# Kernel optimization log

Hardware: AMD Instinct MI355X
Metric: run time of the kernel (lower is better)

## Reference

```python
import jax, jax.numpy as jnp
import numpy as np

BS, L, HIDDEN = 4, 2048, 1024
H, HD, R = 16, 64, 4


def setup_inputs() -> dict:
    key = jax.random.key(0)
    k1, k2, k3, k4 = jax.random.split(key, 4)
    hidden_states = jax.random.normal(k1, (BS, L, HIDDEN), dtype=jnp.float32)
    scale = np.float32(1.0 / np.sqrt(HIDDEN))
    Wk = jax.random.normal(k2, (HIDDEN, H * HD), dtype=jnp.float32) * scale
    bk = jnp.zeros((H * HD,), jnp.float32)
    Wv = jax.random.normal(k3, (HIDDEN, H * HD), dtype=jnp.float32) * scale
    bv = jnp.zeros((H * HD,), jnp.float32)
    xavier = np.float32(np.sqrt(2.0 / (H + HD)))  # xavier_normal_ for (H, HD)
    ReadingHead = jax.random.normal(k4, (H, HD), dtype=jnp.float32) * xavier
    bidirection_weight = jnp.full((H, 2 * R), 1.0 / (2 * R), jnp.float32)
    return dict(hidden_states=hidden_states, Wk=Wk, bk=bk, Wv=Wv, bv=bv,
                ReadingHead=ReadingHead, bidirection_weight=bidirection_weight)


def _shift_step(carry, x):
    # carry: [bs, R, H] int32 registers; x = (valid [bs, H] bool, slot0 scalar int32)
    v, s = x
    bs, r, nh = carry.shape
    shifted = jnp.concatenate([jnp.broadcast_to(s, (bs, 1, nh)).astype(carry.dtype),
                               carry[:, :-1, :]], axis=1)
    new = jnp.where(v[:, None, :], shifted, carry)
    return new, new


def _forward_regs(valid):
    # valid: [bs, L, H] bool -> register index map [bs, L, R, H]
    bs, length, nh = valid.shape
    init = jnp.zeros((bs, R, nh), jnp.int32)  # position 0 registers are 0
    xs = (jnp.moveaxis(valid[:, 1:, :], 1, 0), jnp.arange(1, length, dtype=jnp.int32))
    _, ys = jax.lax.scan(_shift_step, init, xs)
    regs = jnp.concatenate([init[None], ys], axis=0)  # [L, bs, R, H]
    return jnp.moveaxis(regs, 0, 1)


def _backward_regs(valid):
    # valid: [bs, L, H] bool -> register index map [bs, L, R, H]
    bs, length, nh = valid.shape
    last = jnp.where(valid[:, length - 1, :], jnp.int32(length - 1), jnp.int32(0))
    init = jnp.zeros((bs, R, nh), jnp.int32).at[:, 0, :].set(last)  # position L-1
    # scan over positions 1..L-2 in reverse; slot0 at position l is l+1
    xs = (jnp.moveaxis(valid[:, 1:length - 1, :], 1, 0),
          jnp.arange(2, length, dtype=jnp.int32))
    _, ys = jax.lax.scan(_shift_step, init, xs, reverse=True)
    regs = jnp.concatenate([jnp.zeros((1, bs, R, nh), jnp.int32), ys, init[None]], axis=0)
    return jnp.moveaxis(regs, 0, 1)


def _gather_regs(V, regs):
    # V: [bs, L, H, hd]; regs: [bs, L, R, H] -> [bs, H, L, R, hd]
    bs, length, nh, hd = V.shape
    Vt = jnp.moveaxis(V, 2, 1)                       # [bs, H, L, hd]
    idx = jnp.moveaxis(regs, 3, 1).reshape(bs, nh, length * R)
    g = jnp.take_along_axis(Vt, idx[..., None], axis=2)  # [bs, H, L*R, hd]
    return g.reshape(bs, nh, length, R, hd)


def reference(hidden_states, Wk, bk, Wv, bv, ReadingHead, bidirection_weight):
    bs, length, _ = hidden_states.shape
    K1 = jax.nn.relu(hidden_states @ Wk + bk).reshape(bs, length, H, HD)
    V1 = jax.nn.relu(hidden_states @ Wv + bv).reshape(bs, length, H, HD)
    dot = jnp.einsum('blhd,hd->blh', K1, ReadingHead)
    valid = dot > 0.5  # attn_var == 'default' branch
    reg_f = _forward_regs(valid)
    reg_b = _backward_regs(valid)
    Vf = _gather_regs(V1, reg_f)  # [bs, H, L, R, hd]
    Vb = _gather_regs(V1, reg_b)
    out = (jnp.einsum('bhlrd,hr->blhd', Vf, bidirection_weight[:, :R])
           + jnp.einsum('bhlrd,hr->blhd', Vb, bidirection_weight[:, R:]))
    return out.reshape(bs, length, H * HD)
```

## Files before the change

### kernel.cpp

```cpp
#include <hip/hip_runtime.h>
#include <hip/hip_bf16.h>
#include <stdint.h>

#define BS   4
#define LSEQ 2048
#define HID  1024
#define NH   16
#define HD   64
#define M_TOT (BS * LSEQ)
#define NKV   (NH * HD)

typedef __attribute__((ext_vector_type(8))) short short8x;
typedef __attribute__((ext_vector_type(4))) float f32x4;

__device__ __forceinline__ float relu_f(float x) { return x > 0.0f ? x : 0.0f; }

__device__ __forceinline__ ushort bf16_rne(float f) {
    uint32_t x = __float_as_uint(f);
    return (ushort)((x + 0x7FFFu + ((x >> 16) & 1u)) >> 16);
}
__device__ __forceinline__ float bf16_to_f(ushort h) {
    return __uint_as_float((uint32_t)h << 16);
}

__device__ __forceinline__ void gload_lds16(const void* g, void* l) {
    typedef __attribute__((address_space(1))) const uint32_t GU;
    typedef __attribute__((address_space(3))) uint32_t LU;
    __builtin_amdgcn_global_load_lds((GU*)g, (LU*)l, 16, 0, 0);
}


__global__ __launch_bounds__(256) void split_A(const float* __restrict__ A,
                                               ushort* __restrict__ hi,
                                               ushort* __restrict__ lo)
{
    int i = blockIdx.x * 256 + threadIdx.x;
    float4 v = ((const float4*)A)[i];
    ushort4 h, l;
    h.x = bf16_rne(v.x); l.x = bf16_rne(v.x - bf16_to_f(h.x));
    h.y = bf16_rne(v.y); l.y = bf16_rne(v.y - bf16_to_f(h.y));
    h.z = bf16_rne(v.z); l.z = bf16_rne(v.z - bf16_to_f(h.z));
    h.w = bf16_rne(v.w); l.w = bf16_rne(v.w - bf16_to_f(h.w));
    ((ushort4*)hi)[i] = h;
    ((ushort4*)lo)[i] = l;
}

__global__ __launch_bounds__(256) void split_WT(const float* __restrict__ W,
                                                ushort* __restrict__ hiT,
                                                ushort* __restrict__ loT)
{
    __shared__ float t[64][65];
    const int k0 = blockIdx.x * 64, n0 = blockIdx.y * 64;
    const int tid = threadIdx.x;
#pragma unroll
    for (int it = 0; it < 4; ++it) {
        int r = it * 16 + (tid >> 4);
        int c = (tid & 15) * 4;
        float4 v = *(const float4*)&W[(size_t)(k0 + r) * NKV + n0 + c];
        t[r][c] = v.x; t[r][c + 1] = v.y; t[r][c + 2] = v.z; t[r][c + 3] = v.w;
    }
    __syncthreads();
    int n  = tid >> 2;
    int kc = (tid & 3) * 16;
    ushort hb[16], lb[16];
#pragma unroll
    for (int j = 0; j < 16; ++j) {
        float f = t[kc + j][n];
        ushort h = bf16_rne(f);
        hb[j] = h;
        lb[j] = bf16_rne(f - bf16_to_f(h));
    }
    size_t o = (size_t)(n0 + n) * 1024 + k0 + kc;
    *(uint4*)&hiT[o]     = *(uint4*)&hb[0];
    *(uint4*)&hiT[o + 8] = *(uint4*)&hb[8];
    *(uint4*)&loT[o]     = *(uint4*)&lb[0];
    *(uint4*)&loT[o + 8] = *(uint4*)&lb[8];
}

__global__ __launch_bounds__(256, 2) void mfma_gemm(
    const ushort* __restrict__ Ahi, const ushort* __restrict__ Alo,
    const ushort* __restrict__ WvhiT, const ushort* __restrict__ WvloT,
    const ushort* __restrict__ WkhiT, const ushort* __restrict__ WkloT,
    const float* __restrict__ bv, const float* __restrict__ bk,
    const float* __restrict__ RH,
    float* __restrict__ V1, unsigned char* __restrict__ validB)
{
    __shared__ ushort As[128 * 64];
    __shared__ ushort Bsh[128 * 64];

    const int tid  = threadIdx.x;
    const int lane = tid & 63;
    const int wv   = tid >> 6;
    const int wm   = wv >> 1;
    const int wn   = wv & 1;
    const int bm   = blockIdx.x;
    const bool kpath = (blockIdx.y >= 8);
    const int bn   = blockIdx.y & 7;

    const ushort* WT_hi = kpath ? WkhiT : WvhiT;
    const ushort* WT_lo = kpath ? WkloT : WvloT;
    const float*  bias  = kpath ? bk : bv;

    f32x4 acc[4][4];
    const f32x4 z = {0.f, 0.f, 0.f, 0.f};
#pragma unroll
    for (int i = 0; i < 4; ++i)
#pragma unroll
        for (int j = 0; j < 4; ++j) acc[i][j] = z;

    for (int ks = 0; ks < 48; ++ks) {
        const int seg = ks >> 4;
        const int k0  = (ks & 15) << 6;
        const ushort* Aseg = (seg == 1) ? Alo : Ahi;
        const ushort* Wseg = (seg == 2) ? WT_lo : WT_hi;

#pragma unroll
        for (int it = 0; it < 4; ++it) {
            int f = it * 256 + tid;
            int r = f >> 3, c = f & 7;
            const ushort* asrc = Aseg + (size_t)(bm * 128 + r) * 1024 + k0 + ((c ^ (r & 7)) << 3);
            gload_lds16(asrc, &As[(size_t)(it * 256 + wv * 64) * 8]);
        }
#pragma unroll
        for (int it = 0; it < 4; ++it) {
            int f = it * 256 + tid;
            int r = f >> 3, c = f & 7;
            const ushort* bsrc = Wseg + (size_t)(bn * 128 + r) * 1024 + k0 + ((c ^ (r & 7)) << 3);
            gload_lds16(bsrc, &Bsh[(size_t)(it * 256 + wv * 64) * 8]);
        }
        __syncthreads();

        short8x a[4][2], b[4][2];
#pragma unroll
        for (int mi = 0; mi < 4; ++mi)
#pragma unroll
            for (int k2 = 0; k2 < 2; ++k2) {
                int row = wm * 64 + mi * 16 + (lane & 15);
                int ch  = k2 * 4 + (lane >> 4);
                a[mi][k2] = *(const short8x*)((const char*)As + row * 128 + ((ch ^ (row & 7)) << 4));
            }
#pragma unroll
        for (int ni = 0; ni < 4; ++ni)
#pragma unroll
            for (int k2 = 0; k2 < 2; ++k2) {
                int row = wn * 64 + ni * 16 + (lane & 15);
                int ch  = k2 * 4 + (lane >> 4);
                b[ni][k2] = *(const short8x*)((const char*)Bsh + row * 128 + ((ch ^ (row & 7)) << 4));
            }

#pragma unroll
        for (int k2 = 0; k2 < 2; ++k2)
#pragma unroll
            for (int mi = 0; mi < 4; ++mi)
#pragma unroll
                for (int ni = 0; ni < 4; ++ni)
                    acc[mi][ni] = __builtin_amdgcn_mfma_f32_16x16x32_bf16(
                        a[mi][k2], b[ni][k2], acc[mi][ni], 0, 0, 0);
        __syncthreads();
    }

    if (!kpath) {
#pragma unroll
        for (int mi = 0; mi < 4; ++mi)
#pragma unroll
            for (int ni = 0; ni < 4; ++ni) {
                int row0 = bm * 128 + wm * 64 + mi * 16 + (lane >> 4) * 4;
                int col  = bn * 128 + wn * 64 + ni * 16 + (lane & 15);
                float bc = bias[col];
#pragma unroll
                for (int r = 0; r < 4; ++r)
                    V1[(size_t)(row0 + r) * NKV + col] = relu_f(acc[mi][ni][r] + bc);
            }
    } else {
        const int head = bn * 2 + wn;
        float rhw[4], bcs[4];
#pragma unroll
        for (int ni = 0; ni < 4; ++ni) {
            int ch = ni * 16 + (lane & 15);
            rhw[ni] = RH[head * HD + ch];
            bcs[ni] = bias[bn * 128 + wn * 64 + ch];
        }
#pragma unroll
        for (int mi = 0; mi < 4; ++mi) {
            float s[4];
#pragma unroll
            for (int r = 0; r < 4; ++r) {
                float v = 0.f;
#pragma unroll
                for (int ni = 0; ni < 4; ++ni)
                    v += relu_f(acc[mi][ni][r] + bcs[ni]) * rhw[ni];
                s[r] = v;
            }
#pragma unroll
            for (int m = 1; m < 16; m <<= 1)
#pragma unroll
                for (int r = 0; r < 4; ++r)
                    s[r] += __shfl_xor(s[r], m);
            if ((lane & 15) == 0) {
#pragma unroll
                for (int r = 0; r < 4; ++r) {
                    int grow = bm * 128 + wm * 64 + mi * 16 + (lane >> 4) * 4 + r;
                    int bb = grow >> 11, ll = grow & 2047;
                    validB[((size_t)bb * NH + head) * LSEQ + ll] = (s[r] > 0.5f) ? 1 : 0;
                }
            }
        }
    }
}

__global__ __launch_bounds__(256) void scan_kernel(
    const unsigned char* __restrict__ validB,
    short* __restrict__ idxb)
{
    const int bh = blockIdx.x;
    const int b  = bh >> 4;
    const int h  = bh & 15;
    const unsigned char* v = validB + ((size_t)b * NH + h) * LSEQ;

    __shared__ uint64_t words[LSEQ / 64];

    const int tid  = threadIdx.x;
    const int lane = tid & 63;
    const int wv   = tid >> 6;

#pragma unroll
    for (int it = 0; it < LSEQ / 256; ++it) {
        int p = it * 256 + wv * 64 + lane;
        uint64_t m = __ballot(v[p] != 0);
        if (lane == 0) {
            if ((p >> 6) == 0) m &= ~1ull;
            words[p >> 6] = m;
        }
    }
    __syncthreads();

#pragma unroll
    for (int it = 0; it < LSEQ / 256; ++it) {
        int l = it * 256 + tid;
        ushort f[4] = {0, 0, 0, 0};
        ushort g[4] = {0, 0, 0, 0};
        if (l > 0) {
            {
                int wi = l >> 6, bi = l & 63;
                uint64_t m = words[wi] & ((bi == 63) ? ~0ull : ((2ull << bi) - 1));
                int cnt = 0;
                while (cnt < 4) {
                    if (m == 0) { if (wi == 0) break; m = words[--wi]; continue; }
                    int p = 63 - __clzll(m);
                    f[cnt++] = (ushort)(wi * 64 + p);
                    m &= ~(1ull << p);
                }
            }
            {
                int wi = l >> 6, bi = l & 63;
                uint64_t m = words[wi] & (~0ull << bi);
                int cnt = 0;
                while (cnt < 4) {
                    if (m == 0) { if (wi == (LSEQ / 64) - 1) break; m = words[++wi]; continue; }
                    int p = __ffsll((long long)m) - 1;
                    int pos = wi * 64 + p;
                    g[cnt++] = (ushort)((pos >= LSEQ - 1) ? (LSEQ - 1) : (pos + 1));
                    m &= m - 1;
                }
            }
        }
        uint4 pk;
        pk.x = (uint32_t)f[0] | ((uint32_t)f[1] << 16);
        pk.y = (uint32_t)f[2] | ((uint32_t)f[3] << 16);
        pk.z = (uint32_t)g[0] | ((uint32_t)g[1] << 16);
        pk.w = (uint32_t)g[2] | ((uint32_t)g[3] << 16);
        *(uint4*)(idxb + (((size_t)(b * LSEQ + l)) * NH + h) * 8) = pk;
    }
}

__global__ __launch_bounds__(256) void gather_kernel(
    const float* __restrict__ V1,
    const short* __restrict__ idxb,
    const float* __restrict__ bw,
    float* __restrict__ out)
{
    int wid  = (blockIdx.x * 256 + threadIdx.x) >> 6;
    int lane = threadIdx.x & 63;
    int gr   = wid >> 4;
    int h    = wid & 15;
    int b    = gr >> 11;

    const ushort4* ip = (const ushort4*)(idxb + ((size_t)gr * NH + h) * 8);
    ushort4 i0 = ip[0];
    ushort4 i1 = ip[1];

    const float* wp    = bw + h * 8;
    const float* vbase = V1 + (size_t)b * LSEQ * NKV + h * HD + lane;

    float acc = wp[0] * vbase[(size_t)i0.x * NKV] + wp[1] * vbase[(size_t)i0.y * NKV] +
                wp[2] * vbase[(size_t)i0.z * NKV] + wp[3] * vbase[(size_t)i0.w * NKV] +
                wp[4] * vbase[(size_t)i1.x * NKV] + wp[5] * vbase[(size_t)i1.y * NKV] +
                wp[6] * vbase[(size_t)i1.z * NKV] + wp[7] * vbase[(size_t)i1.w * NKV];

    out[(size_t)gr * NKV + h * HD + lane] = acc;
}

extern "C" void kernel_launch(void* const* d_in, const int* in_sizes, int n_in,
                              void* d_out, int out_size, void* d_ws, size_t ws_size,
                              hipStream_t stream)
{
    const float* hs = (const float*)d_in[0];
    const float* Wk = (const float*)d_in[1];
    const float* bk = (const float*)d_in[2];
    const float* Wv = (const float*)d_in[3];
    const float* bv = (const float*)d_in[4];
    const float* RH = (const float*)d_in[5];
    const float* bw = (const float*)d_in[6];
    float* out = (float*)d_out;

    char* ws = (char*)d_ws;
    size_t o = 0;
    float* V1      = (float*)(ws + o);  o += (size_t)M_TOT * NKV * 4;
    ushort* Ahi    = (ushort*)(ws + o); o += (size_t)M_TOT * HID * 2;
    ushort* Alo    = (ushort*)(ws + o); o += (size_t)M_TOT * HID * 2;
    ushort* WvhiT  = (ushort*)(ws + o); o += (size_t)HID * NKV * 2;
    ushort* WvloT  = (ushort*)(ws + o); o += (size_t)HID * NKV * 2;
    ushort* WkhiT  = (ushort*)(ws + o); o += (size_t)HID * NKV * 2;
    ushort* WkloT  = (ushort*)(ws + o); o += (size_t)HID * NKV * 2;
    unsigned char* validB = (unsigned char*)(ws + o); o += (size_t)BS * NH * LSEQ;
    short* idxb    = (short*)(ws + o);  o += (size_t)M_TOT * NH * 8 * 2;

    split_A<<<(M_TOT * HID / 4) / 256, 256, 0, stream>>>(hs, Ahi, Alo);
    split_WT<<<dim3(16, 16), 256, 0, stream>>>(Wv, WvhiT, WvloT);
    split_WT<<<dim3(16, 16), 256, 0, stream>>>(Wk, WkhiT, WkloT);
    mfma_gemm<<<dim3(M_TOT / 128, 16), 256, 0, stream>>>(
        Ahi, Alo, WvhiT, WvloT, WkhiT, WkloT, bv, bk, RH, V1, validB);
    scan_kernel<<<BS * NH, 256, 0, stream>>>(validB, idxb);
    gather_kernel<<<(M_TOT * NH) / 4, 256, 0, stream>>>(V1, idxb, bw, out);
}
```

Measured before the change: 242.9 us.

## Rewrite bf16x3 GEMM as 256x256 double-buffered pipelined kernel; merge split kernels

Each GEMM workgroup now has 512 threads computing a 256x256 tile, up from 128x128. Shared memory is double-buffered, and global-to-LDS loads for the next K step are interleaved with MFMA phases using barriers, setprio and explicit vmcnt waits. This is meant to hide memory latency and raise data reuse per loaded tile. The three split/transpose launches are also folded into a single prep kernel to cut launch overhead. In exchange, LDS use and register pressure rise (acc grows to 8x4 per wave), and the grid shrinks to 256 workgroups, so occupancy and load balance may suffer.

```diff
diff --git a/kernel.cpp b/kernel.cpp
--- a/kernel.cpp
+++ b/kernel.cpp
@@ -9,6 +9,7 @@
 #define HD   64
 #define M_TOT (BS * LSEQ)
 #define NKV   (NH * HD)
+#define NIT   24
 
 typedef __attribute__((ext_vector_type(8))) short short8x;
 typedef __attribute__((ext_vector_type(4))) float f32x4;
@@ -29,55 +30,60 @@
     __builtin_amdgcn_global_load_lds((GU*)g, (LU*)l, 16, 0, 0);
 }
 
-
-__global__ __launch_bounds__(256) void split_A(const float* __restrict__ A,
-                                               ushort* __restrict__ hi,
-                                               ushort* __restrict__ lo)
-{
-    int i = blockIdx.x * 256 + threadIdx.x;
-    float4 v = ((const float4*)A)[i];
-    ushort4 h, l;
-    h.x = bf16_rne(v.x); l.x = bf16_rne(v.x - bf16_to_f(h.x));
-    h.y = bf16_rne(v.y); l.y = bf16_rne(v.y - bf16_to_f(h.y));
-    h.z = bf16_rne(v.z); l.z = bf16_rne(v.z - bf16_to_f(h.z));
-    h.w = bf16_rne(v.w); l.w = bf16_rne(v.w - bf16_to_f(h.w));
-    ((ushort4*)hi)[i] = h;
-    ((ushort4*)lo)[i] = l;
-}
-
-__global__ __launch_bounds__(256) void split_WT(const float* __restrict__ W,
-                                                ushort* __restrict__ hiT,
-                                                ushort* __restrict__ loT)
+__global__ __launch_bounds__(256) void prep(
+    const float* __restrict__ A,
+    const float* __restrict__ Wv, const float* __restrict__ Wk,
+    ushort* __restrict__ Ahi, ushort* __restrict__ Alo,
+    ushort* __restrict__ WvhiT, ushort* __restrict__ WvloT,
+    ushort* __restrict__ WkhiT, ushort* __restrict__ WkloT)
 {
     __shared__ float t[64][65];
-    const int k0 = blockIdx.x * 64, n0 = blockIdx.y * 64;
+    const int bid = blockIdx.x;
     const int tid = threadIdx.x;
-#pragma unroll
-    for (int it = 0; it < 4; ++it) {
-        int r = it * 16 + (tid >> 4);
-        int c = (tid & 15) * 4;
-        float4 v = *(const float4*)&W[(size_t)(k0 + r) * NKV + n0 + c];
-        t[r][c] = v.x; t[r][c + 1] = v.y; t[r][c + 2] = v.z; t[r][c + 3] = v.w;
+    if (bid < 8192) {
+        int i = bid * 256 + tid;
+        float4 v = ((const float4*)A)[i];
+        ushort4 h, l;
+        h.x = bf16_rne(v.x); l.x = bf16_rne(v.x - bf16_to_f(h.x));
+        h.y = bf16_rne(v.y); l.y = bf16_rne(v.y - bf16_to_f(h.y));
+        h.z = bf16_rne(v.z); l.z = bf16_rne(v.z - bf16_to_f(h.z));
+        h.w = bf16_rne(v.w); l.w = bf16_rne(v.w - bf16_to_f(h.w));
+        ((ushort4*)Ahi)[i] = h;
+        ((ushort4*)Alo)[i] = l;
+    } else {
+        int idx = bid - 8192;
+        const float* W  = (idx < 256) ? Wv : Wk;
+        ushort* hiT     = (idx < 256) ? WvhiT : WkhiT;
+        ushort* loT     = (idx < 256) ? WvloT : WkloT;
+        int tt = idx & 255;
+        int k0 = (tt >> 4) * 64, n0 = (tt & 15) * 64;
+#pragma unroll
+        for (int it = 0; it < 4; ++it) {
+            int r = it * 16 + (tid >> 4);
+            int c = (tid & 15) * 4;
+            float4 v = *(const float4*)&W[(size_t)(k0 + r) * NKV + n0 + c];
+            t[r][c] = v.x; t[r][c + 1] = v.y; t[r][c + 2] = v.z; t[r][c + 3] = v.w;
+        }
+        __syncthreads();
+        int n  = tid >> 2;
+        int kc = (tid & 3) * 16;
+        ushort hb[16], lb[16];
+#pragma unroll
+        for (int j = 0; j < 16; ++j) {
+            float f = t[kc + j][n];
+            ushort h = bf16_rne(f);
+            hb[j] = h;
+            lb[j] = bf16_rne(f - bf16_to_f(h));
+        }
+        size_t o = (size_t)(n0 + n) * 1024 + k0 + kc;
+        *(uint4*)&hiT[o]     = *(uint4*)&hb[0];
+        *(uint4*)&hiT[o + 8] = *(uint4*)&hb[8];
+        *(uint4*)&loT[o]     = *(uint4*)&lb[0];
+        *(uint4*)&loT[o + 8] = *(uint4*)&lb[8];
     }
-    __syncthreads();
-    int n  = tid >> 2;
-    int kc = (tid & 3) * 16;
-    ushort hb[16], lb[16];
-#pragma unroll
-    for (int j = 0; j < 16; ++j) {
-        float f = t[kc + j][n];
-        ushort h = bf16_rne(f);
-        hb[j] = h;
-        lb[j] = bf16_rne(f - bf16_to_f(h));
-    }
-    size_t o = (size_t)(n0 + n) * 1024 + k0 + kc;
-    *(uint4*)&hiT[o]     = *(uint4*)&hb[0];
-    *(uint4*)&hiT[o + 8] = *(uint4*)&hb[8];
-    *(uint4*)&loT[o]     = *(uint4*)&lb[0];
-    *(uint4*)&loT[o + 8] = *(uint4*)&lb[8];
-}
-
-__global__ __launch_bounds__(256, 2) void mfma_gemm(
+}
+
+__global__ __launch_bounds__(512, 2) void mfma_gemm(
     const ushort* __restrict__ Ahi, const ushort* __restrict__ Alo,
     const ushort* __restrict__ WvhiT, const ushort* __restrict__ WvloT,
     const ushort* __restrict__ WkhiT, const ushort* __restrict__ WkloT,
@@ -85,103 +91,199 @@
     const float* __restrict__ RH,
     float* __restrict__ V1, unsigned char* __restrict__ validB)
 {
-    __shared__ ushort As[128 * 64];
-    __shared__ ushort Bsh[128 * 64];
+    __shared__ ushort LA[2][256 * 64];
+    __shared__ ushort LB[2][256 * 64];
 
     const int tid  = threadIdx.x;
     const int lane = tid & 63;
     const int wv   = tid >> 6;
-    const int wm   = wv >> 1;
-    const int wn   = wv & 1;
+    const int wm   = wv >> 2;
+    const int wn   = wv & 3;
     const int bm   = blockIdx.x;
-    const bool kpath = (blockIdx.y >= 8);
-    const int bn   = blockIdx.y & 7;
-
-    const ushort* WT_hi = kpath ? WkhiT : WvhiT;
-    const ushort* WT_lo = kpath ? WkloT : WvloT;
-    const float*  bias  = kpath ? bk : bv;
-
-    f32x4 acc[4][4];
-    const f32x4 z = {0.f, 0.f, 0.f, 0.f};
-#pragma unroll
-    for (int i = 0; i < 4; ++i)
-#pragma unroll
-        for (int j = 0; j < 4; ++j) acc[i][j] = z;
-
-    for (int ks = 0; ks < 48; ++ks) {
-        const int seg = ks >> 4;
-        const int k0  = (ks & 15) << 6;
-        const ushort* Aseg = (seg == 1) ? Alo : Ahi;
-        const ushort* Wseg = (seg == 2) ? WT_lo : WT_hi;
-
-#pragma unroll
-        for (int it = 0; it < 4; ++it) {
-            int f = it * 256 + tid;
-            int r = f >> 3, c = f & 7;
-            const ushort* asrc = Aseg + (size_t)(bm * 128 + r) * 1024 + k0 + ((c ^ (r & 7)) << 3);
-            gload_lds16(asrc, &As[(size_t)(it * 256 + wv * 64) * 8]);
-        }
-#pragma unroll
-        for (int it = 0; it < 4; ++it) {
-            int f = it * 256 + tid;
-            int r = f >> 3, c = f & 7;
-            const ushort* bsrc = Wseg + (size_t)(bn * 128 + r) * 1024 + k0 + ((c ^ (r & 7)) << 3);
-            gload_lds16(bsrc, &Bsh[(size_t)(it * 256 + wv * 64) * 8]);
-        }
-        __syncthreads();
-
-        short8x a[4][2], b[4][2];
-#pragma unroll
-        for (int mi = 0; mi < 4; ++mi)
-#pragma unroll
-            for (int k2 = 0; k2 < 2; ++k2) {
-                int row = wm * 64 + mi * 16 + (lane & 15);
-                int ch  = k2 * 4 + (lane >> 4);
-                a[mi][k2] = *(const short8x*)((const char*)As + row * 128 + ((ch ^ (row & 7)) << 4));
-            }
-#pragma unroll
-        for (int ni = 0; ni < 4; ++ni)
-#pragma unroll
-            for (int k2 = 0; k2 < 2; ++k2) {
-                int row = wn * 64 + ni * 16 + (lane & 15);
-                int ch  = k2 * 4 + (lane >> 4);
-                b[ni][k2] = *(const short8x*)((const char*)Bsh + row * 128 + ((ch ^ (row & 7)) << 4));
-            }
-
-#pragma unroll
-        for (int k2 = 0; k2 < 2; ++k2)
-#pragma unroll
-            for (int mi = 0; mi < 4; ++mi)
-#pragma unroll
-                for (int ni = 0; ni < 4; ++ni)
-                    acc[mi][ni] = __builtin_amdgcn_mfma_f32_16x16x32_bf16(
-                        a[mi][k2], b[ni][k2], acc[mi][ni], 0, 0, 0);
-        __syncthreads();
+    const bool kpath = (blockIdx.y >= 4);
+    const int bnl  = kpath ? (blockIdx.y - 4) : blockIdx.y;
+
+    const ushort* Whi  = kpath ? WkhiT : WvhiT;
+    const ushort* Wlo  = kpath ? WkloT : WvloT;
+    const float*  bias = kpath ? bk : bv;
+
+    f32x4 acc[8][4];
+    const f32x4 zz = {0.f, 0.f, 0.f, 0.f};
+#pragma unroll
+    for (int i = 0; i < 8; ++i)
+#pragma unroll
+        for (int j = 0; j < 4; ++j) acc[i][j] = zz;
+
+    const int rc0 = ((0 + (lane >> 4)) ^ (lane & 7)) * 8;
+    const int rc1 = ((4 + (lane >> 4)) ^ (lane & 7)) * 8;
+
+    auto Asrc = [&](int kt, int half) -> const ushort* {
+        const ushort* base = ((kt >> 4) == 1) ? Alo : Ahi;
+        return base + (size_t)(bm * 256 + half * 128) * 1024 + ((kt & 15) << 6);
+    };
+    auto Bsrc = [&](int kt, int half) -> const ushort* {
+        const ushort* base = ((kt >> 4) == 2) ? Wlo : Whi;
+        return base + (size_t)(bnl * 256 + half * 128) * 1024 + ((kt & 15) << 6);
+    };
+
+#define STAGE_HALF(dst, src) do {                                              \
+    _Pragma("unroll")                                                          \
+    for (int it_ = 0; it_ < 2; ++it_) {                                        \
+        int f_ = it_ * 512 + tid;                                              \
+        int r_ = f_ >> 3, c_ = f_ & 7;                                         \
+        gload_lds16((src) + (size_t)r_ * 1024 + ((c_ ^ (r_ & 7)) << 3),        \
+                    (dst) + (size_t)(it_ * 512 + wv * 64) * 8);                \
+    }                                                                          \
+} while (0)
+
+#define READ_A(buf, half) do {                                                 \
+    _Pragma("unroll")                                                          \
+    for (int mi_ = 0; mi_ < 4; ++mi_) {                                        \
+        int row_ = wm * 128 + (half) * 64 + mi_ * 16 + (lane & 15);            \
+        const ushort* b_ = &LA[buf][row_ * 64];                                \
+        a_f[mi_][0] = *(const short8x*)(b_ + rc0);                             \
+        a_f[mi_][1] = *(const short8x*)(b_ + rc1);                             \
+    }                                                                          \
+} while (0)
+
+#define READ_B(buf, half) do {                                                 \
+    _Pragma("unroll")                                                          \
+    for (int nj_ = 0; nj_ < 2; ++nj_) {                                        \
+        int ni_ = (half) * 2 + nj_;                                            \
+        int row_ = wn * 64 + ni_ * 16 + (lane & 15);                           \
+        const ushort* b_ = &LB[buf][row_ * 64];                                \
+        b_f[ni_][0] = *(const short8x*)(b_ + rc0);                             \
+        b_f[ni_][1] = *(const short8x*)(b_ + rc1);                             \
+    }                                                                          \
+} while (0)
+
+#define MFMA_QUAD(mh, nh) do {                                                 \
+    _Pragma("unroll")                                                          \
+    for (int k2_ = 0; k2_ < 2; ++k2_)                                          \
+        _Pragma("unroll")                                                      \
+        for (int mi_ = 0; mi_ < 4; ++mi_)                                      \
+            _Pragma("unroll")                                                  \
+            for (int nj_ = 0; nj_ < 2; ++nj_) {                                \
+                int ni_ = (nh) * 2 + nj_;                                      \
+                acc[(mh) * 4 + mi_][ni_] =                                     \
+                    __builtin_amdgcn_mfma_f32_16x16x32_bf16(                   \
+                        a_f[mi_][k2_], b_f[ni_][k2_], acc[(mh) * 4 + mi_][ni_],\
+                        0, 0, 0);                                              \
+            }                                                                  \
+} while (0)
+
+#define PHASE_SYNC()                                                           \
+    __builtin_amdgcn_s_barrier();                                              \
+    asm volatile("s_waitcnt lgkmcnt(0)" ::: "memory");                         \
+    __builtin_amdgcn_sched_barrier(0);                                         \
+    __builtin_amdgcn_s_setprio(1)
+
+#define PHASE_END()                                                            \
+    __builtin_amdgcn_s_setprio(0);                                             \
+    __builtin_amdgcn_s_barrier()
+
+    short8x a_f[4][2], b_f[4][2];
+
+    STAGE_HALF(&LA[0][0],    Asrc(0, 0));
+    STAGE_HALF(&LA[0][8192], Asrc(0, 1));
+    STAGE_HALF(&LB[0][0],    Bsrc(0, 0));
+    STAGE_HALF(&LB[0][8192], Bsrc(0, 1));
+    STAGE_HALF(&LA[1][0],    Asrc(1, 0));
+    STAGE_HALF(&LA[1][8192], Asrc(1, 1));
+    STAGE_HALF(&LB[1][0],    Bsrc(1, 0));
+    STAGE_HALF(&LB[1][8192], Bsrc(1, 1));
+    asm volatile("s_waitcnt vmcnt(8)" ::: "memory");
+    __builtin_amdgcn_s_barrier();
+
+#pragma unroll 1
+    for (int i = 0; i < NIT; ++i) {
+        const int kt0 = 2 * i;
+        const int kt1 = 2 * i + 1;
+        const bool st = (i < NIT - 1);
+
+        READ_A(0, 0); READ_B(0, 0);
+        PHASE_SYNC();
+        MFMA_QUAD(0, 0);
+        PHASE_END();
+
+        READ_B(0, 1);
+        PHASE_SYNC();
+        MFMA_QUAD(0, 1);
+        PHASE_END();
+
+        READ_A(0, 1);
+        if (st) {
+            STAGE_HALF(&LB[0][0],    Bsrc(kt0 + 2, 0));
+            STAGE_HALF(&LB[0][8192], Bsrc(kt0 + 2, 1));
+        }
+        PHASE_SYNC();
+        MFMA_QUAD(1, 1);
+        PHASE_END();
+
+        if (st) {
+            STAGE_HALF(&LA[0][0],    Asrc(kt0 + 2, 0));
+            STAGE_HALF(&LA[0][8192], Asrc(kt0 + 2, 1));
+        }
+        PHASE_SYNC();
+        MFMA_QUAD(1, 0);
+        __builtin_amdgcn_s_setprio(0);
+        if (st) asm volatile("s_waitcnt vmcnt(8)" ::: "memory");
+        else    asm volatile("s_waitcnt vmcnt(0)" ::: "memory");
+        __builtin_amdgcn_s_barrier();
+
+        READ_A(1, 0); READ_B(1, 0);
+        PHASE_SYNC();
+        MFMA_QUAD(0, 0);
+        PHASE_END();
+
+        READ_B(1, 1);
+        PHASE_SYNC();
+        MFMA_QUAD(0, 1);
+        PHASE_END();
+
+        READ_A(1, 1);
+        if (st) {
+            STAGE_HALF(&LB[1][0],    Bsrc(kt1 + 2, 0));
+            STAGE_HALF(&LB[1][8192], Bsrc(kt1 + 2, 1));
+        }
+        PHASE_SYNC();
+        MFMA_QUAD(1, 1);
+        PHASE_END();
+
+        if (st) {
+            STAGE_HALF(&LA[1][0],    Asrc(kt1 + 2, 1 - 1));
+            STAGE_HALF(&LA[1][8192], Asrc(kt1 + 2, 1));
+        }
+        PHASE_SYNC();
+        MFMA_QUAD(1, 0);
+        __builtin_amdgcn_s_setprio(0);
+        if (st) asm volatile("s_waitcnt vmcnt(8)" ::: "memory");
+        __builtin_amdgcn_s_barrier();
     }
 
     if (!kpath) {
 #pragma unroll
-        for (int mi = 0; mi < 4; ++mi)
+        for (int mi = 0; mi < 8; ++mi)
 #pragma unroll
             for (int ni = 0; ni < 4; ++ni) {
-                int row0 = bm * 128 + wm * 64 + mi * 16 + (lane >> 4) * 4;
-                int col  = bn * 128 + wn * 64 + ni * 16 + (lane & 15);
+                int row0 = bm * 256 + wm * 128 + mi * 16 + (lane >> 4) * 4;
+                int col  = bnl * 256 + wn * 64 + ni * 16 + (lane & 15);
                 float bc = bias[col];
 #pragma unroll
                 for (int r = 0; r < 4; ++r)
                     V1[(size_t)(row0 + r) * NKV + col] = relu_f(acc[mi][ni][r] + bc);
             }
     } else {
-        const int head = bn * 2 + wn;
+        const int head = bnl * 4 + wn;
         float rhw[4], bcs[4];
 #pragma unroll
         for (int ni = 0; ni < 4; ++ni) {
             int ch = ni * 16 + (lane & 15);
             rhw[ni] = RH[head * HD + ch];
-            bcs[ni] = bias[bn * 128 + wn * 64 + ch];
-        }
-#pragma unroll
-        for (int mi = 0; mi < 4; ++mi) {
+            bcs[ni] = bias[head * HD + ch];
+        }
+#pragma unroll
+        for (int mi = 0; mi < 8; ++mi) {
             float s[4];
 #pragma unroll
             for (int r = 0; r < 4; ++r) {
@@ -199,13 +301,19 @@
             if ((lane & 15) == 0) {
 #pragma unroll
                 for (int r = 0; r < 4; ++r) {
-                    int grow = bm * 128 + wm * 64 + mi * 16 + (lane >> 4) * 4 + r;
+                    int grow = bm * 256 + wm * 128 + mi * 16 + (lane >> 4) * 4 + r;
                     int bb = grow >> 11, ll = grow & 2047;
                     validB[((size_t)bb * NH + head) * LSEQ + ll] = (s[r] > 0.5f) ? 1 : 0;
                 }
             }
         }
     }
+#undef STAGE_HALF
+#undef READ_A
+#undef READ_B
+#undef MFMA_QUAD
+#undef PHASE_SYNC
+#undef PHASE_END
 }
 
 __global__ __launch_bounds__(256) void scan_kernel(
@@ -325,10 +433,9 @@
     unsigned char* validB = (unsigned char*)(ws + o); o += (size_t)BS * NH * LSEQ;
     short* idxb    = (short*)(ws + o);  o += (size_t)M_TOT * NH * 8 * 2;
 
-    split_A<<<(M_TOT * HID / 4) / 256, 256, 0, stream>>>(hs, Ahi, Alo);
-    split_WT<<<dim3(16, 16), 256, 0, stream>>>(Wv, WvhiT, WvloT);
-    split_WT<<<dim3(16, 16), 256, 0, stream>>>(Wk, WkhiT, WkloT);
-    mfma_gemm<<<dim3(M_TOT / 128, 16), 256, 0, stream>>>(
+    prep<<<8192 + 512, 256, 0, stream>>>(hs, Wv, Wk, Ahi, Alo,
+                                         WvhiT, WvloT, WkhiT, WkloT);
+    mfma_gemm<<<dim3(M_TOT / 256, 8), 512, 0, stream>>>(
         Ahi, Alo, WvhiT, WvloT, WkhiT, WkloT, bv, bk, RH, V1, validB);
     scan_kernel<<<BS * NH, 256, 0, stream>>>(validB, idxb);
     gather_kernel<<<(M_TOT * NH) / 4, 256, 0, stream>>>(V1, idxb, bw, out);
```

Measured after the change: 228.2 us. 1.06x faster.
